# Kernel tuning notes

Measured on AMD Instinct MI355X. Metric: run time of the kernel, lower is better.

## Reference

```python
import jax, jax.numpy as jnp
import numpy as np

# (dv=3, dc=6)-regular Tanner graph: M checks, N=2M vars, E=M*dc edges
M, N, DV, DC, D, B, T = 1024, 2048, 3, 6, 8, 128, 5
CIN = DC * D          # check-MLP in/out dim = 48
VIN = DV * D + 1      # var-MLP in/out dim  = 25 (extra scalar = LLR)
HC, HV = 4 * CIN, 4 * VIN
EPS = 1e-6


def _graph():
    # variable j connects to checks (j + l) % M, l = 0..DV-1 -> every check has degree DC
    var_nbrs = (np.arange(N)[:, None] + np.arange(DV)[None, :]) % M   # [N, DV] check ids
    # var-edge id e = j*DV + l ; sort edges by check to get check-slot ordering
    order = np.argsort(var_nbrs.reshape(-1), kind='stable')           # check-edge p -> var-edge e
    chk_nbrs = (order // DV).reshape(M, DC)                           # var id in each check slot
    inv_order = np.argsort(order)                                     # var-edge e -> check-edge p
    return chk_nbrs, order, inv_order


def setup_inputs() -> dict:
    key = jax.random.key(0)
    ks = jax.random.split(key, 12)
    chk_nbrs, order, inv_order = _graph()
    prior = np.clip(np.random.default_rng(0).uniform(0.005, 0.05, size=N), EPS, 1 - EPS)
    prior_llr = jnp.asarray(np.log((1.0 - prior) / prior), jnp.float32)

    def lin_w(k, g, nin, nout):
        return jax.random.normal(k, (g, nin, nout), jnp.float32) / np.sqrt(nin)

    def lin_b(k, g, nout):
        return 0.02 * jax.random.normal(k, (g, nout), jnp.float32)

    return {
        "syndromes": jax.random.randint(ks[0], (B, M), 0, 2, jnp.int32),
        "prior_llr": prior_llr,
        "chk_w1": lin_w(ks[1], M, CIN, HC), "chk_b1": lin_b(ks[2], M, HC),
        "chk_w2": lin_w(ks[3], M, HC, CIN), "chk_b2": lin_b(ks[4], M, CIN),
        "var_w1": lin_w(ks[5], N, VIN, HV), "var_b1": lin_b(ks[6], N, HV),
        "var_w2": lin_w(ks[7], N, HV, VIN), "var_b2": lin_b(ks[8], N, VIN),
        "chk_nbrs": jnp.asarray(chk_nbrs, jnp.int32),      # [M, DC] var id per check slot
        "c2v_gather": jnp.asarray(inv_order, jnp.int32),   # var-edge -> check-edge perm
        "v2c_gather": jnp.asarray(order, jnp.int32),       # check-edge -> var-edge perm
    }


def reference(syndromes, prior_llr, chk_w1, chk_b1, chk_w2, chk_b2,
              var_w1, var_b1, var_w2, var_b2, chk_nbrs, c2v_gather, v2c_gather):
    synd_sgn = (1 - 2 * syndromes).astype(jnp.float32)                    # [B, M]
    prior_b = jnp.broadcast_to(prior_llr, (B, N))[..., None]              # [B, N, 1]

    def chk_mlp(x):  # x: [B, M, CIN], per-check grouped GEMM
        h = jax.nn.gelu(jnp.einsum('bmi,mih->bmh', x, chk_w1) + chk_b1, approximate=False)
        return jnp.einsum('bmh,mho->bmo', h, chk_w2) + chk_b2

    def var_mlp(x):  # x: [B, N, VIN]
        h = jax.nn.gelu(jnp.einsum('bni,nih->bnh', x, var_w1) + var_b1, approximate=False)
        return jnp.einsum('bnh,nho->bno', h, var_w2) + var_b2

    # init check in-messages: zeros with first component = prior LLR of neighbor var
    chk_in = jnp.zeros((B, M, DC, D), jnp.float32).at[..., 0].set(prior_llr[chk_nbrs][None])

    def step(chk_in, _):
        y = chk_mlp(chk_in.reshape(B, M, CIN)).reshape(B, M, DC, D)
        y = y * synd_sgn[:, :, None, None]                                # syndrome sign flip
        var_in = y.reshape(B, M * DC, D)[:, c2v_gather]                   # scatter c->v as gather
        x = jnp.concatenate([var_in.reshape(B, N, DV * D), prior_b], axis=-1)
        out = var_mlp(x)
        llr = out[..., DV * D]                                            # [B, N]
        msg = out[..., :DV * D].reshape(B, N * DV, D)
        chk_in_new = msg[:, v2c_gather].reshape(B, M, DC, D)              # scatter v->c as gather
        return chk_in_new, llr

    _, llrs = jax.lax.scan(step, chk_in, None, length=T)
    return llrs  # [T, B, N]
```

## Files before the change

### kernel.cpp

```cpp
#include <hip/hip_runtime.h>
#include <math.h>

#define MM 1024
#define NN 2048
#define BB 128
#define TT 5
#define EE 6144

typedef __bf16 bf16x8 __attribute__((ext_vector_type(8)));
typedef __bf16 bf16x4 __attribute__((ext_vector_type(4)));
typedef short  s16x4  __attribute__((ext_vector_type(4)));
typedef float  f32x4  __attribute__((ext_vector_type(4)));
typedef unsigned int u32x4 __attribute__((ext_vector_type(4)));

#define CHK_W_ELEMS 22272
#define CHK_L2_OFF  12288
#define VAR_W_ELEMS 7168
#define VAR_L2_OFF  3584

__device__ __forceinline__ float gelu_fast(float x) {
    float xe = x * 0.70710678118654752f;
    float ax = fabsf(xe);
    float t  = __builtin_amdgcn_rcpf(1.0f + 0.3275911f * ax);
    float p  = t * (0.254829592f + t * (-0.284496736f + t * (1.421413741f +
               t * (-1.453152027f + t * 1.061405429f))));
    float er = 1.0f - p * __expf(-xe * xe);
    er = copysignf(er, xe);
    return 0.5f * x * (1.0f + er);
}

__device__ __forceinline__ f32x4 mfma16(bf16x4 a, bf16x4 b, f32x4 c) {
#if __has_builtin(__builtin_amdgcn_mfma_f32_16x16x16bf16_1k)
    return __builtin_amdgcn_mfma_f32_16x16x16bf16_1k(
        __builtin_bit_cast(s16x4, a), __builtin_bit_cast(s16x4, b), c, 0, 0, 0);
#else
    f32x4 d;
    asm volatile("v_mfma_f32_16x16x16_bf16 %0, %1, %2, %3\n\ts_nop 4"
                 : "=v"(d) : "v"(a), "v"(b), "v"(c));
    return d;
#endif
}

__device__ __forceinline__ void wave_lds_fence() {
    asm volatile("s_waitcnt lgkmcnt(0)" ::: "memory");
}

__global__ __launch_bounds__(256)
void init_kernel(const float* __restrict__ prior, __bf16* __restrict__ v2c)
{
    int idx = blockIdx.x * 256 + threadIdx.x;
    int e = idx >> 7;
    bf16x8 v;
    #pragma unroll
    for (int j = 0; j < 8; ++j) v[j] = (__bf16)0.0f;
    v[0] = (__bf16)prior[e / 3];
    *(bf16x8*)(v2c + (size_t)idx * 8) = v;
}

__global__ __launch_bounds__(256)
void sgn_kernel(const int* __restrict__ synd, float* __restrict__ sgnT)
{
    int idx = blockIdx.x * 256 + threadIdx.x;
    int m = idx >> 7, b = idx & 127;
    sgnT[idx] = (float)(1 - 2 * synd[(size_t)b * MM + m]);
}

__global__ __launch_bounds__(256)
void prep_all(const float* __restrict__ cw1, const float* __restrict__ cb1,
              const float* __restrict__ cw2, const float* __restrict__ cb2,
              const float* __restrict__ vw1, const float* __restrict__ vb1,
              const float* __restrict__ vw2, const float* __restrict__ vb2,
              __bf16* __restrict__ wchk, __bf16* __restrict__ wvar)
{
    const int wid = blockIdx.x * 4 + (threadIdx.x >> 6);
    const int l = threadIdx.x & 63, q = l >> 4, c = l & 15;

    if (wid < 24576) {
        const int m = wid / 24, f = wid % 24;
        const int mt = f >> 1, kt = f & 1;
        const int h = mt * 16 + c;
        const float* s1 = cw1 + (size_t)m * (48 * 192);
        float tmp[8];
        #pragma unroll
        for (int j = 0; j < 8; ++j) {
            int k = kt * 32 + q * 8 + j;
            tmp[j] = s1[min(k, 47) * 192 + h];
        }
        float bv = cb1[(size_t)m * 192 + h];
        bf16x8 v;
        #pragma unroll
        for (int j = 0; j < 8; ++j) {
            int k = kt * 32 + q * 8 + j;
            float x = (k < 48) ? tmp[j] : ((k == 48) ? bv : 0.0f);
            v[j] = (__bf16)x;
        }
        *(bf16x8*)(wchk + (size_t)m * CHK_W_ELEMS + f * 512 + l * 8) = v;
    } else if (wid < 37888) {
        const int t = wid - 24576;
        const int m = t / 13, ks = t % 13;
        __bf16* base = wchk + (size_t)m * CHK_W_ELEMS + CHK_L2_OFF;
        if (ks < 12) {
            const float* s2 = cw2 + (size_t)m * (192 * 48);
            #pragma unroll
            for (int mt = 0; mt < 3; ++mt) {
                const int o = mt * 16 + c;
                bf16x4 v;
                #pragma unroll
                for (int i = 0; i < 4; ++i)
                    v[i] = (__bf16)s2[(ks * 16 + q * 4 + i) * 48 + o];
                *(bf16x4*)(base + (ks * 3 + mt) * 256 + l * 4) = v;
            }
        } else {
            #pragma unroll
            for (int mt = 0; mt < 3; ++mt) {
                const int o = mt * 16 + c;
                float bv = cb2[(size_t)m * 48 + o];
                bf16x4 v;
                #pragma unroll
                for (int i = 0; i < 4; ++i) v[i] = (__bf16)0.0f;
                if (q == 0) v[0] = (__bf16)bv;
                *(bf16x4*)(base + (12 * 3 + mt) * 256 + l * 4) = v;
            }
        }
    } else if (wid < 52224) {
        const int t = wid - 37888;
        const int nv = t / 7, mt = t % 7;
        const int h = mt * 16 + c, hc = min(h, 99);
        const float* s1 = vw1 + (size_t)nv * (25 * 100);
        float tmp[8];
        #pragma unroll
        for (int j = 0; j < 8; ++j)
            tmp[j] = s1[min(q * 8 + j, 24) * 100 + hc];
        float bv = vb1[(size_t)nv * 100 + hc];
        bf16x8 v;
        #pragma unroll
        for (int j = 0; j < 8; ++j) {
            int k = q * 8 + j;
            float x = 0.0f;
            if (h < 100) x = (k < 25) ? tmp[j] : ((k == 25) ? bv : 0.0f);
            v[j] = (__bf16)x;
        }
        *(bf16x8*)(wvar + (size_t)nv * VAR_W_ELEMS + mt * 512 + l * 8) = v;
    } else {
        const int t = wid - 52224;
        const int nv = t / 7, ks = t % 7;
        const float* s2 = vw2 + (size_t)nv * (100 * 25);
        __bf16* base = wvar + (size_t)nv * VAR_W_ELEMS + VAR_L2_OFF;
        #pragma unroll
        for (int mt = 0; mt < 2; ++mt) {
            const int o = mt * 16 + c, oc = min(o, 24);
            float tmp[4];
            #pragma unroll
            for (int i = 0; i < 4; ++i)
                tmp[i] = s2[min(ks * 16 + q * 4 + i, 99) * 25 + oc];
            float bv = vb2[(size_t)nv * 25 + oc];
            bf16x4 v;
            #pragma unroll
            for (int i = 0; i < 4; ++i) {
                int k = ks * 16 + q * 4 + i;
                float x = 0.0f;
                if (o < 25) x = (k < 100) ? tmp[i] : ((k == 100) ? bv : 0.0f);
                v[i] = (__bf16)x;
            }
            *(bf16x4*)(base + (ks * 2 + mt) * 256 + l * 4) = v;
        }
    }
}

#define CPITCH 58
__global__ __launch_bounds__(256, 3)
void chk_kernel(const __bf16* __restrict__ wchk,
                const float* __restrict__ sgnT,
                const int* __restrict__ v2c_gather,
                const __bf16* __restrict__ v2c, __bf16* __restrict__ c2v)
{
    const int m = blockIdx.x;
    const int tid = threadIdx.x;
    const int w = tid >> 6, l = tid & 63, q = l >> 4, c = l & 15;

    __shared__ __align__(16) __bf16 wlds[CHK_W_ELEMS];
    __shared__ __align__(16) __bf16 ytile[4 * 16 * CPITCH];
    {
        const __bf16* src = wchk + (size_t)m * CHK_W_ELEMS;
        for (int i = tid; i < CHK_W_ELEMS / 8; i += 256)
            *(u32x4*)(wlds + i * 8) = *(const u32x4*)(src + i * 8);
    }
    const int e0 = v2c_gather[m * 6 + q];
    const int e1 = (q < 2) ? v2c_gather[m * 6 + 4 + q] : 0;
    __syncthreads();

    __bf16* myy = ytile + w * 16 * CPITCH;

    for (int t2 = 0; t2 < 2; ++t2) {
        const int bt = t2 * 64 + w * 16;

        bf16x8 b0 = *(const bf16x8*)(v2c + ((size_t)e0 * BB + bt + c) * 8);
        bf16x8 b1f;
        #pragma unroll
        for (int j = 0; j < 8; ++j) b1f[j] = (__bf16)0.0f;
        if (q < 2)       b1f = *(const bf16x8*)(v2c + ((size_t)e1 * BB + bt + c) * 8);
        else if (q == 2) b1f[0] = (__bf16)1.0f;

        f32x4 acc[12];
        #pragma unroll
        for (int mt = 0; mt < 12; ++mt) {
            bf16x8 a0 = *(const bf16x8*)(wlds + (mt * 2 + 0) * 512 + l * 8);
            bf16x8 a1 = *(const bf16x8*)(wlds + (mt * 2 + 1) * 512 + l * 8);
            f32x4 z = {0.f, 0.f, 0.f, 0.f};
            z = __builtin_amdgcn_mfma_f32_16x16x32_bf16(a0, b0, z, 0, 0, 0);
            z = __builtin_amdgcn_mfma_f32_16x16x32_bf16(a1, b1f, z, 0, 0, 0);
            acc[mt] = z;
        }

        f32x4 acc2[3];
        #pragma unroll
        for (int mt = 0; mt < 3; ++mt) acc2[mt] = (f32x4){0.f, 0.f, 0.f, 0.f};
        #pragma unroll
        for (int ks = 0; ks < 13; ++ks) {
            bf16x4 bf;
            if (ks < 12) {
                #pragma unroll
                for (int r = 0; r < 4; ++r) bf[r] = (__bf16)gelu_fast(acc[ks][r]);
            } else {
                #pragma unroll
                for (int r = 0; r < 4; ++r) bf[r] = (__bf16)0.0f;
                if (q == 0) bf[0] = (__bf16)1.0f;
            }
            #pragma unroll
            for (int mt = 0; mt < 3; ++mt) {
                bf16x4 af = *(const bf16x4*)(wlds + CHK_L2_OFF + (ks * 3 + mt) * 256 + l * 4);
                acc2[mt] = mfma16(af, bf, acc2[mt]);
            }
        }

        const float sg = sgnT[m * BB + bt + c];
        #pragma unroll
        for (int mt = 0; mt < 3; ++mt)
            #pragma unroll
            for (int r = 0; r < 4; ++r)
                myy[c * CPITCH + mt * 16 + q * 4 + r] = (__bf16)(acc2[mt][r] * sg);
        wave_lds_fence();

        {
            int s = l >> 4, row = l & 15;
            u32x4 vv = *(const u32x4*)(myy + row * CPITCH + s * 8);
            *(u32x4*)(c2v + ((size_t)(m * 6 + s) * BB + bt + row) * 8) = vv;
            if (l < 32) {
                int s2 = 4 + (l >> 4), row2 = l & 15;
                u32x4 v2 = *(const u32x4*)(myy + row2 * CPITCH + s2 * 8);
                *(u32x4*)(c2v + ((size_t)(m * 6 + s2) * BB + bt + row2) * 8) = v2;
            }
        }
        wave_lds_fence();
    }
}

#define VPITCH 26
__global__ __launch_bounds__(256, 4)
void var_kernel(const __bf16* __restrict__ wvar,
                const int* __restrict__ c2v_gather, const float* __restrict__ prior,
                const __bf16* __restrict__ c2v, __bf16* __restrict__ v2c,
                float* __restrict__ llr_out, int last)
{
    const int nv = blockIdx.x;
    const int tid = threadIdx.x;
    const int w = tid >> 6, l = tid & 63, q = l >> 4, c = l & 15;

    __shared__ __align__(16) __bf16 wlds[VAR_W_ELEMS];
    __shared__ __align__(16) __bf16 ytile[4 * 16 * VPITCH];
    {
        const __bf16* src = wvar + (size_t)nv * VAR_W_ELEMS;
        for (int i = tid; i < VAR_W_ELEMS / 8; i += 256)
            *(u32x4*)(wlds + i * 8) = *(const u32x4*)(src + i * 8);
    }
    const int ep = (q < 3) ? c2v_gather[nv * 3 + q] : 0;
    const __bf16 prbf = (__bf16)prior[nv];
    __syncthreads();

    __bf16* myy = ytile + w * 16 * VPITCH;

    for (int t2 = 0; t2 < 2; ++t2) {
        const int bt = t2 * 64 + w * 16;

        bf16x8 b0;
        #pragma unroll
        for (int j = 0; j < 8; ++j) b0[j] = (__bf16)0.0f;
        if (q < 3) b0 = *(const bf16x8*)(c2v + ((size_t)ep * BB + bt + c) * 8);
        else { b0[0] = prbf; b0[1] = (__bf16)1.0f; }

        f32x4 acc[7];
        #pragma unroll
        for (int mt = 0; mt < 7; ++mt) {
            bf16x8 a0 = *(const bf16x8*)(wlds + mt * 512 + l * 8);
            f32x4 z = {0.f, 0.f, 0.f, 0.f};
            acc[mt] = __builtin_amdgcn_mfma_f32_16x16x32_bf16(a0, b0, z, 0, 0, 0);
        }

        f32x4 acc2[2];
        acc2[0] = (f32x4){0.f, 0.f, 0.f, 0.f};
        acc2[1] = (f32x4){0.f, 0.f, 0.f, 0.f};
        #pragma unroll
        for (int ks = 0; ks < 7; ++ks) {
            bf16x4 bf;
            #pragma unroll
            for (int r = 0; r < 4; ++r) bf[r] = (__bf16)gelu_fast(acc[ks][r]);
            if (ks == 6 && q == 1) bf[0] = (__bf16)1.0f;
            #pragma unroll
            for (int mt = 0; mt < 2; ++mt) {
                bf16x4 af = *(const bf16x4*)(wlds + VAR_L2_OFF + (ks * 2 + mt) * 256 + l * 4);
                acc2[mt] = mfma16(af, bf, acc2[mt]);
            }
        }

        #pragma unroll
        for (int r = 0; r < 4; ++r)
            myy[c * VPITCH + q * 4 + r] = (__bf16)acc2[0][r];
        if (q < 2)
            #pragma unroll
            for (int r = 0; r < 4; ++r)
                myy[c * VPITCH + 16 + q * 4 + r] = (__bf16)acc2[1][r];
        if (q == 2) llr_out[(size_t)(bt + c) * NN + nv] = acc2[1][0];
        wave_lds_fence();

        if (!last && l < 48) {
            int s = l >> 4, row = l & 15;
            u32x4 vv = *(const u32x4*)(myy + row * VPITCH + s * 8);
            *(u32x4*)(v2c + ((size_t)(nv * 3 + s) * BB + bt + row) * 8) = vv;
        }
        wave_lds_fence();
    }
}

extern "C" void kernel_launch(void* const* d_in, const int* in_sizes, int n_in,
                              void* d_out, int out_size, void* d_ws, size_t ws_size,
                              hipStream_t stream) {
    const int*   syndromes = (const int*)  d_in[0];
    const float* prior_llr = (const float*)d_in[1];
    const float* chk_w1    = (const float*)d_in[2];
    const float* chk_b1    = (const float*)d_in[3];
    const float* chk_w2    = (const float*)d_in[4];
    const float* chk_b2    = (const float*)d_in[5];
    const float* var_w1    = (const float*)d_in[6];
    const float* var_b1    = (const float*)d_in[7];
    const float* var_w2    = (const float*)d_in[8];
    const float* var_b2    = (const float*)d_in[9];
    const int*   c2v_g     = (const int*)  d_in[11];
    const int*   v2c_g     = (const int*)  d_in[12];

    float* out = (float*)d_out;

    __bf16* v2c  = (__bf16*)d_ws;
    __bf16* c2v  = v2c + (size_t)EE * BB * 8;
    __bf16* wchk = c2v + (size_t)EE * BB * 8;
    __bf16* wvar = wchk + (size_t)MM * CHK_W_ELEMS;
    float*  sgnT = (float*)(wvar + (size_t)NN * VAR_W_ELEMS);

    prep_all<<<16640, 256, 0, stream>>>(chk_w1, chk_b1, chk_w2, chk_b2,
                                        var_w1, var_b1, var_w2, var_b2,
                                        wchk, wvar);
    sgn_kernel<<<MM * BB / 256, 256, 0, stream>>>(syndromes, sgnT);
    init_kernel<<<EE * BB / 256, 256, 0, stream>>>(prior_llr, v2c);

    for (int t = 0; t < TT; ++t) {
        chk_kernel<<<MM, 256, 0, stream>>>(wchk, sgnT, v2c_g, v2c, c2v);
        var_kernel<<<NN, 256, 0, stream>>>(wvar, c2v_g, prior_llr, c2v, v2c,
                                           out + (size_t)t * BB * NN,
                                           (t == TT - 1) ? 1 : 0);
    }
}
```

Measured before the change: 402.0 us.

## Fuse weight prep, sign and init kernels; stage weights via coalesced LDS loads

Merges the three setup kernels into one launch. Each block now handles a whole per-node weight matrix, loading it from global memory into LDS with coalesced float4 reads before writing the MFMA-tiled bf16 layout from shared memory. This replaces the old strided per-element global gathers. The cost is heavy LDS use in the check branch (about 73 KB per block), which limits how many blocks can be resident at once.

```diff
diff --git a/kernel.cpp b/kernel.cpp
--- a/kernel.cpp
+++ b/kernel.cpp
@@ -45,125 +45,151 @@
     asm volatile("s_waitcnt lgkmcnt(0)" ::: "memory");
 }
 
+#define PREP_GRID (1024 + 2048 + 512 + 3072)
+
 __global__ __launch_bounds__(256)
-void init_kernel(const float* __restrict__ prior, __bf16* __restrict__ v2c)
+void prep_fused(const float* __restrict__ cw1, const float* __restrict__ cb1,
+                const float* __restrict__ cw2, const float* __restrict__ cb2,
+                const float* __restrict__ vw1, const float* __restrict__ vb1,
+                const float* __restrict__ vw2, const float* __restrict__ vb2,
+                const int* __restrict__ synd, const float* __restrict__ prior,
+                __bf16* __restrict__ wchk, __bf16* __restrict__ wvar,
+                float* __restrict__ sgnT, __bf16* __restrict__ v2c)
 {
-    int idx = blockIdx.x * 256 + threadIdx.x;
-    int e = idx >> 7;
-    bf16x8 v;
-    #pragma unroll
-    for (int j = 0; j < 8; ++j) v[j] = (__bf16)0.0f;
-    v[0] = (__bf16)prior[e / 3];
-    *(bf16x8*)(v2c + (size_t)idx * 8) = v;
-}
-
-__global__ __launch_bounds__(256)
-void sgn_kernel(const int* __restrict__ synd, float* __restrict__ sgnT)
-{
-    int idx = blockIdx.x * 256 + threadIdx.x;
-    int m = idx >> 7, b = idx & 127;
-    sgnT[idx] = (float)(1 - 2 * synd[(size_t)b * MM + m]);
-}
-
-__global__ __launch_bounds__(256)
-void prep_all(const float* __restrict__ cw1, const float* __restrict__ cb1,
-              const float* __restrict__ cw2, const float* __restrict__ cb2,
-              const float* __restrict__ vw1, const float* __restrict__ vb1,
-              const float* __restrict__ vw2, const float* __restrict__ vb2,
-              __bf16* __restrict__ wchk, __bf16* __restrict__ wvar)
-{
-    const int wid = blockIdx.x * 4 + (threadIdx.x >> 6);
-    const int l = threadIdx.x & 63, q = l >> 4, c = l & 15;
-
-    if (wid < 24576) {
-        const int m = wid / 24, f = wid % 24;
-        const int mt = f >> 1, kt = f & 1;
-        const int h = mt * 16 + c;
-        const float* s1 = cw1 + (size_t)m * (48 * 192);
-        float tmp[8];
-        #pragma unroll
-        for (int j = 0; j < 8; ++j) {
-            int k = kt * 32 + q * 8 + j;
-            tmp[j] = s1[min(k, 47) * 192 + h];
-        }
-        float bv = cb1[(size_t)m * 192 + h];
+    const int bid = blockIdx.x;
+    const int tid = threadIdx.x;
+
+    __shared__ __align__(16) float s[18672];
+
+    if (bid < 1024) {
+        const int m = bid;
+        {
+            const float4* g1 = (const float4*)(cw1 + (size_t)m * 9216);
+            const float4* g2 = (const float4*)(cw2 + (size_t)m * 9216);
+            float4* s4 = (float4*)s;
+            #pragma unroll
+            for (int it = 0; it < 9; ++it) s4[it * 256 + tid] = g1[it * 256 + tid];
+            #pragma unroll
+            for (int it = 0; it < 9; ++it) s4[2304 + it * 256 + tid] = g2[it * 256 + tid];
+            if (tid < 192) s[18432 + tid] = cb1[(size_t)m * 192 + tid];
+            if (tid < 48)  s[18624 + tid] = cb2[(size_t)m * 48 + tid];
+        }
+        __syncthreads();
+
+        __bf16* dst = wchk + (size_t)m * CHK_W_ELEMS;
+
+        #pragma unroll
+        for (int it = 0; it < 6; ++it) {
+            int i = it * 256 + tid;
+            int l = i & 63, f = i >> 6;
+            int mt = f >> 1, kt = f & 1, q = l >> 4, c = l & 15;
+            int h = mt * 16 + c;
+            bf16x8 v;
+            #pragma unroll
+            for (int j = 0; j < 8; ++j) {
+                int k  = kt * 32 + q * 8 + j;
+                int kc = min(k, 47);
+                float wv = s[kc * 192 + h];
+                float x  = (k < 48) ? wv : ((k == 48) ? s[18432 + h] : 0.0f);
+                v[j] = (__bf16)x;
+            }
+            *(bf16x8*)(dst + i * 8) = v;
+        }
+        #pragma unroll
+        for (int it = 0; it < 10; ++it) {
+            int i = it * 256 + tid;
+            if (i < 2496) {
+                int l = i & 63, f = i >> 6;
+                int ks = f / 3, mt = f - ks * 3;
+                int q = l >> 4, c = l & 15, o = mt * 16 + c;
+                bf16x4 v;
+                #pragma unroll
+                for (int r = 0; r < 4; ++r) {
+                    int k  = ks * 16 + q * 4 + r;
+                    int kc = min(k, 191);
+                    float wv = s[9216 + kc * 48 + o];
+                    float x  = (k < 192) ? wv : ((k == 192) ? s[18624 + o] : 0.0f);
+                    v[r] = (__bf16)x;
+                }
+                *(bf16x4*)(dst + CHK_L2_OFF + i * 4) = v;
+            }
+        }
+    } else if (bid < 3072) {
+        const int nv = bid - 1024;
+        {
+            const float4* g1 = (const float4*)(vw1 + (size_t)nv * 2500);
+            const float4* g2 = (const float4*)(vw2 + (size_t)nv * 2500);
+            float4* s4 = (float4*)s;
+            #pragma unroll
+            for (int it = 0; it < 3; ++it) {
+                int i = it * 256 + tid;
+                if (i < 625) s4[i] = g1[i];
+            }
+            #pragma unroll
+            for (int it = 0; it < 3; ++it) {
+                int i = it * 256 + tid;
+                if (i < 625) s4[625 + i] = g2[i];
+            }
+            if (tid < 100) s[5000 + tid] = vb1[(size_t)nv * 100 + tid];
+            if (tid < 25)  s[5100 + tid] = vb2[(size_t)nv * 25 + tid];
+        }
+        __syncthreads();
+
+        __bf16* dst = wvar + (size_t)nv * VAR_W_ELEMS;
+
+        #pragma unroll
+        for (int it = 0; it < 2; ++it) {
+            int i = it * 256 + tid;
+            if (i < 448) {
+                int l = i & 63, mt = i >> 6;
+                int q = l >> 4, c = l & 15, h = mt * 16 + c;
+                int hc = min(h, 99);
+                bf16x8 v;
+                #pragma unroll
+                for (int j = 0; j < 8; ++j) {
+                    int k  = q * 8 + j;
+                    int kc = min(k, 24);
+                    float wv = s[kc * 100 + hc];
+                    float x = 0.0f;
+                    if (h < 100) x = (k < 25) ? wv : ((k == 25) ? s[5000 + h] : 0.0f);
+                    v[j] = (__bf16)x;
+                }
+                *(bf16x8*)(dst + i * 8) = v;
+            }
+        }
+        #pragma unroll
+        for (int it = 0; it < 4; ++it) {
+            int i = it * 256 + tid;
+            if (i < 896) {
+                int l = i & 63, f = i >> 6;
+                int ks = f >> 1, mt = f & 1;
+                int q = l >> 4, c = l & 15, o = mt * 16 + c;
+                int oc = min(o, 24);
+                bf16x4 v;
+                #pragma unroll
+                for (int r = 0; r < 4; ++r) {
+                    int k  = ks * 16 + q * 4 + r;
+                    int kc = min(k, 99);
+                    float wv = s[2500 + kc * 25 + oc];
+                    float x = 0.0f;
+                    if (o < 25) x = (k < 100) ? wv : ((k == 100) ? s[5100 + o] : 0.0f);
+                    v[r] = (__bf16)x;
+                }
+                *(bf16x4*)(dst + VAR_L2_OFF + i * 4) = v;
+            }
+        }
+    } else if (bid < 3584) {
+        int idx = (bid - 3072) * 256 + tid;
+        int m = idx >> 7, b = idx & 127;
+        sgnT[idx] = (float)(1 - 2 * synd[(size_t)b * MM + m]);
+    } else {
+        int idx = (bid - 3584) * 256 + tid;
+        int e = idx >> 7;
         bf16x8 v;
         #pragma unroll
-        for (int j = 0; j < 8; ++j) {
-            int k = kt * 32 + q * 8 + j;
-            float x = (k < 48) ? tmp[j] : ((k == 48) ? bv : 0.0f);
-            v[j] = (__bf16)x;
-        }
-        *(bf16x8*)(wchk + (size_t)m * CHK_W_ELEMS + f * 512 + l * 8) = v;
-    } else if (wid < 37888) {
-        const int t = wid - 24576;
-        const int m = t / 13, ks = t % 13;
-        __bf16* base = wchk + (size_t)m * CHK_W_ELEMS + CHK_L2_OFF;
-        if (ks < 12) {
-            const float* s2 = cw2 + (size_t)m * (192 * 48);
-            #pragma unroll
-            for (int mt = 0; mt < 3; ++mt) {
-                const int o = mt * 16 + c;
-                bf16x4 v;
-                #pragma unroll
-                for (int i = 0; i < 4; ++i)
-                    v[i] = (__bf16)s2[(ks * 16 + q * 4 + i) * 48 + o];
-                *(bf16x4*)(base + (ks * 3 + mt) * 256 + l * 4) = v;
-            }
-        } else {
-            #pragma unroll
-            for (int mt = 0; mt < 3; ++mt) {
-                const int o = mt * 16 + c;
-                float bv = cb2[(size_t)m * 48 + o];
-                bf16x4 v;
-                #pragma unroll
-                for (int i = 0; i < 4; ++i) v[i] = (__bf16)0.0f;
-                if (q == 0) v[0] = (__bf16)bv;
-                *(bf16x4*)(base + (12 * 3 + mt) * 256 + l * 4) = v;
-            }
-        }
-    } else if (wid < 52224) {
-        const int t = wid - 37888;
-        const int nv = t / 7, mt = t % 7;
-        const int h = mt * 16 + c, hc = min(h, 99);
-        const float* s1 = vw1 + (size_t)nv * (25 * 100);
-        float tmp[8];
-        #pragma unroll
-        for (int j = 0; j < 8; ++j)
-            tmp[j] = s1[min(q * 8 + j, 24) * 100 + hc];
-        float bv = vb1[(size_t)nv * 100 + hc];
-        bf16x8 v;
-        #pragma unroll
-        for (int j = 0; j < 8; ++j) {
-            int k = q * 8 + j;
-            float x = 0.0f;
-            if (h < 100) x = (k < 25) ? tmp[j] : ((k == 25) ? bv : 0.0f);
-            v[j] = (__bf16)x;
-        }
-        *(bf16x8*)(wvar + (size_t)nv * VAR_W_ELEMS + mt * 512 + l * 8) = v;
-    } else {
-        const int t = wid - 52224;
-        const int nv = t / 7, ks = t % 7;
-        const float* s2 = vw2 + (size_t)nv * (100 * 25);
-        __bf16* base = wvar + (size_t)nv * VAR_W_ELEMS + VAR_L2_OFF;
-        #pragma unroll
-        for (int mt = 0; mt < 2; ++mt) {
-            const int o = mt * 16 + c, oc = min(o, 24);
-            float tmp[4];
-            #pragma unroll
-            for (int i = 0; i < 4; ++i)
-                tmp[i] = s2[min(ks * 16 + q * 4 + i, 99) * 25 + oc];
-            float bv = vb2[(size_t)nv * 25 + oc];
-            bf16x4 v;
-            #pragma unroll
-            for (int i = 0; i < 4; ++i) {
-                int k = ks * 16 + q * 4 + i;
-                float x = 0.0f;
-                if (o < 25) x = (k < 100) ? tmp[i] : ((k == 100) ? bv : 0.0f);
-                v[i] = (__bf16)x;
-            }
-            *(bf16x4*)(base + (ks * 2 + mt) * 256 + l * 4) = v;
-        }
+        for (int j = 0; j < 8; ++j) v[j] = (__bf16)0.0f;
+        v[0] = (__bf16)prior[e / 3];
+        *(bf16x8*)(v2c + (size_t)idx * 8) = v;
     }
 }
 
@@ -355,11 +381,10 @@
     __bf16* wvar = wchk + (size_t)MM * CHK_W_ELEMS;
     float*  sgnT = (float*)(wvar + (size_t)NN * VAR_W_ELEMS);
 
-    prep_all<<<16640, 256, 0, stream>>>(chk_w1, chk_b1, chk_w2, chk_b2,
-                                        var_w1, var_b1, var_w2, var_b2,
-                                        wchk, wvar);
-    sgn_kernel<<<MM * BB / 256, 256, 0, stream>>>(syndromes, sgnT);
-    init_kernel<<<EE * BB / 256, 256, 0, stream>>>(prior_llr, v2c);
+    prep_fused<<<PREP_GRID, 256, 0, stream>>>(chk_w1, chk_b1, chk_w2, chk_b2,
+                                              var_w1, var_b1, var_w2, var_b2,
+                                              syndromes, prior_llr,
+                                              wchk, wvar, sgnT, v2c);
 
     for (int t = 0; t < TT; ++t) {
         chk_kernel<<<MM, 256, 0, stream>>>(wchk, sgnT, v2c_g, v2c, c2v);
```

After: 424.0 us. +5.5%, slower.
